# Performance work log

Hardware: AMD Instinct MI355X
Metric: run time of the kernel (lower is better)

The kernel has to match this reference:

```python
import jax, jax.numpy as jnp
import numpy as np

B, S, D, H = 4, 2048, 1024, 16
DEPTH = D // H  # 64


def setup_inputs() -> dict:
    key = jax.random.key(0)
    ks = jax.random.split(key, 11)
    scale = 1.0 / np.sqrt(D)
    inp = {
        "v": jax.random.normal(ks[0], (B, S, D), jnp.float32),
        "k": jax.random.normal(ks[1], (B, S, D), jnp.float32),
        "q": jax.random.normal(ks[2], (B, S, D), jnp.float32),
        # causal mask: 1.0 where attention is disallowed (strict upper triangle)
        "mask": jnp.triu(jnp.ones((S, S), jnp.float32), k=1)[None, None, :, :],
        "wq": jax.random.normal(ks[3], (D, D), jnp.float32) * scale,
        "bq": jnp.zeros((D,), jnp.float32),
        "wk": jax.random.normal(ks[4], (D, D), jnp.float32) * scale,
        "bk": jnp.zeros((D,), jnp.float32),
        "wv": jax.random.normal(ks[5], (D, D), jnp.float32) * scale,
        "bv": jnp.zeros((D,), jnp.float32),
        "wo": jax.random.normal(ks[6], (D, D), jnp.float32) * scale,
        "bo": jnp.zeros((D,), jnp.float32),
    }
    return inp


def _split_heads(x):
    # [B, S, D] -> [B, H, S, depth]
    b, s, _ = x.shape
    return x.reshape(b, s, H, DEPTH).transpose(0, 2, 1, 3)


def reference(v, k, q, mask, wq, bq, wk, bk, wv, bv, wo, bo):
    qh = _split_heads(q @ wq + bq)  # [B,H,S,depth]
    kh = _split_heads(k @ wk + bk)
    vh = _split_heads(v @ wv + bv)

    logits = jnp.einsum("bhqd,bhkd->bhqk", qh, kh) / jnp.sqrt(
        jnp.asarray(DEPTH, jnp.float32)
    )
    logits = logits + mask * -1e9
    attn = jax.nn.softmax(logits, axis=-1)  # [B,H,S,S]
    out = jnp.einsum("bhqk,bhkd->bhqd", attn, vh)
    out = out.transpose(0, 2, 1, 3).reshape(q.shape[0], -1, D)  # [B,S,D]
    return out @ wo + bo
```

## Files before the change

kernel.cpp:

```cpp
#include <hip/hip_runtime.h>

typedef _Float16 f16;
typedef _Float16 half8 __attribute__((ext_vector_type(8)));
typedef _Float16 half4v __attribute__((ext_vector_type(4)));
typedef _Float16 half2v __attribute__((ext_vector_type(2)));
typedef float f32x4 __attribute__((ext_vector_type(4)));

__device__ __forceinline__ void gl_lds16(const void* g, void* l) {
    __builtin_amdgcn_global_load_lds((const __attribute__((address_space(1))) void*)g,
                                     (__attribute__((address_space(3))) void*)l, 16, 0, 0);
}

__device__ __forceinline__ unsigned pack_f16(float a, float b) {
    union { half2v h; unsigned u; } un;
    un.h[0] = (f16)a; un.h[1] = (f16)b;
    return un.u;
}

__device__ __forceinline__ void prep_w_body(const float* __restrict__ W, f16* __restrict__ Wt)
{
    __shared__ float t[64][65];
    const int tid = threadIdx.x;
    const int tk = blockIdx.x * 64, tn = blockIdx.y * 64;
    const int rr = tid >> 4, cc = (tid & 15) * 4;
    #pragma unroll
    for (int j = 0; j < 4; ++j) {
        float4 v = *(const float4*)(W + (size_t)(tk + rr + j * 16) * 1024 + tn + cc);
        t[rr + j * 16][cc] = v.x; t[rr + j * 16][cc + 1] = v.y;
        t[rr + j * 16][cc + 2] = v.z; t[rr + j * 16][cc + 3] = v.w;
    }
    __syncthreads();
    const int n = tid >> 2, kc = (tid & 3) * 16;
    f16 o[16];
    #pragma unroll
    for (int j = 0; j < 16; ++j) o[j] = (f16)t[kc + j][n];
    f16* dst = Wt + (size_t)(tn + n) * 1024 + tk + kc;
    *(uint4*)dst = *(uint4*)o;
    *(uint4*)(dst + 8) = *(uint4*)(o + 8);
}

__global__ __launch_bounds__(256) void prep_w1(const float* __restrict__ W, f16* __restrict__ Wt)
{ prep_w_body(W, Wt); }

__global__ __launch_bounds__(256) void prep_w3(const float* __restrict__ w0,
    const float* __restrict__ w1, const float* __restrict__ w2, f16* __restrict__ Wt)
{
    const int z = blockIdx.z;
    const float* W = (z == 0) ? w0 : (z == 1) ? w1 : w2;
    prep_w_body(W, Wt + (size_t)z * 1024 * 1024);
}

__global__ __launch_bounds__(512, 2) void qkv_gemm(
    const float* __restrict__ Xq, const float* __restrict__ Xk, const float* __restrict__ Xv,
    const f16* __restrict__ Wt,
    const float* __restrict__ bqp, const float* __restrict__ bkp, const float* __restrict__ bvp,
    f16* __restrict__ qh, f16* __restrict__ kh, f16* __restrict__ vth)
{
    __shared__ __align__(16) f16 As[2][256 * 64];
    __shared__ __align__(16) f16 Bs[2][256 * 64];

    const int z = blockIdx.z;
    const float* X    = (z == 0) ? Xq : (z == 1) ? Xk : Xv;
    const float* bias = (z == 0) ? bqp : (z == 1) ? bkp : bvp;
    const f16*   W    = Wt + (size_t)z * 1024 * 1024;

    const int tid = threadIdx.x;
    const int lane = tid & 63;
    const int lane16 = lane & 15, quad = lane >> 4;
    const int wave = tid >> 6;
    const int wm = (wave & 1) * 128;
    const int wn = (wave >> 1) * 64;

    const int lin = blockIdx.x + 4 * blockIdx.y;
    const int xcd = lin & 7, t = lin >> 3;
    const int m0 = (((t >> 2) << 3) | xcd) * 256;
    const int n0 = (t & 3) * 256;

    const int srow = tid >> 3;
    const int sch  = tid & 7;
    const int swc  = sch ^ (srow & 7);

    const size_t xgbase = (size_t)(m0 + srow) * 1024 + sch * 8;
    const size_t wgbase = (size_t)(n0 + srow) * 1024 + swc * 8;
    const int wldsbase = (tid & 448) * 8;

    f32x4 acc[8][4] = {};

    {
        float4 xr[4][2];
        #pragma unroll
        for (int i = 0; i < 4; ++i) {
            xr[i][0] = *(const float4*)(X + xgbase + (size_t)i * 65536);
            xr[i][1] = *(const float4*)(X + xgbase + (size_t)i * 65536 + 4);
        }
        #pragma unroll
        for (int i = 0; i < 4; ++i)
            gl_lds16(W + wgbase + (size_t)i * 65536, Bs[0] + i * 4096 + wldsbase);
        asm volatile("s_waitcnt vmcnt(4)" ::: "memory");
        #pragma unroll
        for (int i = 0; i < 4; ++i) {
            half8 hx;
            hx[0] = (f16)xr[i][0].x; hx[1] = (f16)xr[i][0].y;
            hx[2] = (f16)xr[i][0].z; hx[3] = (f16)xr[i][0].w;
            hx[4] = (f16)xr[i][1].x; hx[5] = (f16)xr[i][1].y;
            hx[6] = (f16)xr[i][1].z; hx[7] = (f16)xr[i][1].w;
            *(half8*)(As[0] + i * 4096 + srow * 64 + swc * 8) = hx;
        }
        asm volatile("s_waitcnt vmcnt(0) lgkmcnt(0)" ::: "memory");
        __builtin_amdgcn_s_barrier();
        asm volatile("" ::: "memory");
    }

    for (int kt = 0; kt < 16; ++kt) {
        const int cur = kt & 1, nb = cur ^ 1;
        const bool pf = (kt + 1 < 16);
        const f16* Ab = As[cur];
        const f16* Bb = Bs[cur];

        float4 xr[4][2];
        if (pf) {
            const float* xs = X + xgbase + (kt + 1) * 64;
            #pragma unroll
            for (int i = 0; i < 4; ++i) {
                xr[i][0] = *(const float4*)(xs + (size_t)i * 65536);
                xr[i][1] = *(const float4*)(xs + (size_t)i * 65536 + 4);
            }
        }
        half8 af0[4][2], bf[4][2];
        #pragma unroll
        for (int i = 0; i < 4; ++i) {
            const int ra = wm + i * 16 + lane16;
            const int rb = wn + i * 16 + lane16;
            #pragma unroll
            for (int c = 0; c < 2; ++c) {
                af0[i][c] = *(const half8*)(Ab + ra * 64 + (((c * 4 + quad) ^ (ra & 7)) * 8));
                bf[i][c]  = *(const half8*)(Bb + rb * 64 + (((c * 4 + quad) ^ (rb & 7)) * 8));
            }
        }
        asm volatile("s_waitcnt lgkmcnt(0)" ::: "memory");
        __builtin_amdgcn_s_setprio(1);
        #pragma unroll
        for (int c = 0; c < 2; ++c)
            #pragma unroll
            for (int mi = 0; mi < 4; ++mi)
                #pragma unroll
                for (int ni = 0; ni < 4; ++ni)
                    acc[mi][ni] = __builtin_amdgcn_mfma_f32_16x16x32_f16(af0[mi][c], bf[ni][c], acc[mi][ni], 0, 0, 0);
        __builtin_amdgcn_s_setprio(0);
        asm volatile("" ::: "memory");
        __builtin_amdgcn_s_barrier();
        asm volatile("" ::: "memory");

        half8 af1[4][2];
        #pragma unroll
        for (int i = 0; i < 4; ++i) {
            const int ra = wm + 64 + i * 16 + lane16;
            #pragma unroll
            for (int c = 0; c < 2; ++c)
                af1[i][c] = *(const half8*)(Ab + ra * 64 + (((c * 4 + quad) ^ (ra & 7)) * 8));
        }
        if (pf) {
            const f16* ws = W + wgbase + (kt + 1) * 64;
            #pragma unroll
            for (int i = 0; i < 4; ++i)
                gl_lds16(ws + (size_t)i * 65536, Bs[nb] + i * 4096 + wldsbase);
            asm volatile("s_waitcnt vmcnt(4)" ::: "memory");
            #pragma unroll
            for (int i = 0; i < 4; ++i) {
                half8 hx;
                hx[0] = (f16)xr[i][0].x; hx[1] = (f16)xr[i][0].y;
                hx[2] = (f16)xr[i][0].z; hx[3] = (f16)xr[i][0].w;
                hx[4] = (f16)xr[i][1].x; hx[5] = (f16)xr[i][1].y;
                hx[6] = (f16)xr[i][1].z; hx[7] = (f16)xr[i][1].w;
                *(half8*)(As[nb] + i * 4096 + srow * 64 + swc * 8) = hx;
            }
        }
        asm volatile("s_waitcnt lgkmcnt(0)" ::: "memory");
        __builtin_amdgcn_s_setprio(1);
        #pragma unroll
        for (int c = 0; c < 2; ++c)
            #pragma unroll
            for (int mi = 0; mi < 4; ++mi)
                #pragma unroll
                for (int ni = 0; ni < 4; ++ni)
                    acc[4 + mi][ni] = __builtin_amdgcn_mfma_f32_16x16x32_f16(af1[mi][c], bf[ni][c], acc[4 + mi][ni], 0, 0, 0);
        __builtin_amdgcn_s_setprio(0);
        if (pf) asm volatile("s_waitcnt vmcnt(0)" ::: "memory");
        asm volatile("" ::: "memory");
        __builtin_amdgcn_s_barrier();
        asm volatile("" ::: "memory");
    }

    #pragma unroll
    for (int mi = 0; mi < 8; ++mi) {
        #pragma unroll
        for (int ni = 0; ni < 4; ++ni) {
            const int col = n0 + wn + ni * 16 + lane16;
            const float bval = bias[col];
            const int grow0 = m0 + wm + mi * 16 + quad * 4;
            if (z == 2) {
                const int b = grow0 >> 11, s0 = grow0 & 2047;
                const int h = col >> 6, d = col & 63;
                half4v p;
                #pragma unroll
                for (int r = 0; r < 4; ++r) p[r] = (f16)(acc[mi][ni][r] + bval);
                *(half4v*)(vth + (((size_t)b * 16 + h) * 64 + d) * 2048 + s0) = p;
            } else {
                f16* out = (z == 0) ? qh : kh;
                #pragma unroll
                for (int r = 0; r < 4; ++r)
                    out[(size_t)(grow0 + r) * 1024 + col] = (f16)(acc[mi][ni][r] + bval);
            }
        }
    }
}

__global__ __launch_bounds__(256, 2) void out_gemm(
    const f16* __restrict__ X, const f16* __restrict__ Wt,
    const float* __restrict__ bias, float* __restrict__ out)
{
    __shared__ __align__(16) f16 As[2][128 * 64];
    __shared__ __align__(16) f16 Bs[2][128 * 64];

    const int tid = threadIdx.x;
    const int lane = tid & 63;
    const int lane16 = lane & 15, quad = lane >> 4;
    const int wave = tid >> 6;
    const int wm = (wave >> 1) * 64, wn = (wave & 1) * 64;

    const int lin = blockIdx.x + 8 * blockIdx.y;
    const int xcd = lin & 7, t = lin >> 3;
    const int m0 = ((t >> 3) * 8 + xcd) * 128;
    const int n0 = (t & 7) * 128;

    const int wbase = tid & 192;
    const int srow = tid >> 3, schunk = tid & 7;
    const int swc = schunk ^ (srow & 7);

    f32x4 acc[4][4] = {};

    #pragma unroll
    for (int i = 0; i < 4; ++i) {
        gl_lds16(Wt + (size_t)(n0 + i * 32 + srow) * 1024 + swc * 8, Bs[0] + (size_t)(i * 256 + wbase) * 8);
        gl_lds16(X  + (size_t)(m0 + i * 32 + srow) * 1024 + swc * 8, As[0] + (size_t)(i * 256 + wbase) * 8);
    }

    for (int kt = 0; kt < 16; ++kt) {
        if (kt + 1 < 16) {
            const int nb = (kt + 1) & 1;
            const int k1 = (kt + 1) * 64;
            #pragma unroll
            for (int i = 0; i < 4; ++i) {
                gl_lds16(Wt + (size_t)(n0 + i * 32 + srow) * 1024 + k1 + swc * 8, Bs[nb] + (size_t)(i * 256 + wbase) * 8);
                gl_lds16(X  + (size_t)(m0 + i * 32 + srow) * 1024 + k1 + swc * 8, As[nb] + (size_t)(i * 256 + wbase) * 8);
            }
            asm volatile("s_waitcnt vmcnt(8)" ::: "memory");
        } else {
            asm volatile("s_waitcnt vmcnt(0)" ::: "memory");
        }
        __builtin_amdgcn_s_barrier();
        asm volatile("" ::: "memory");

        const f16* Ab = As[kt & 1];
        const f16* Bb = Bs[kt & 1];
        half8 af[4][2], bf[4][2];
        #pragma unroll
        for (int i = 0; i < 4; ++i) {
            const int ra = wm + i * 16 + lane16;
            const int rb = wn + i * 16 + lane16;
            #pragma unroll
            for (int c = 0; c < 2; ++c) {
                af[i][c] = *(const half8*)(Ab + ra * 64 + (((c * 4 + quad) ^ (ra & 7)) * 8));
                bf[i][c] = *(const half8*)(Bb + rb * 64 + (((c * 4 + quad) ^ (rb & 7)) * 8));
            }
        }
        #pragma unroll
        for (int c = 0; c < 2; ++c)
            #pragma unroll
            for (int mi = 0; mi < 4; ++mi)
                #pragma unroll
                for (int ni = 0; ni < 4; ++ni)
                    acc[mi][ni] = __builtin_amdgcn_mfma_f32_16x16x32_f16(af[mi][c], bf[ni][c], acc[mi][ni], 0, 0, 0);

        asm volatile("" ::: "memory");
        __builtin_amdgcn_s_barrier();
        asm volatile("" ::: "memory");
    }

    #pragma unroll
    for (int mi = 0; mi < 4; ++mi) {
        #pragma unroll
        for (int ni = 0; ni < 4; ++ni) {
            const int col = n0 + wn + ni * 16 + lane16;
            const float bval = bias[col];
            const int grow0 = m0 + wm + mi * 16 + quad * 4;
            #pragma unroll
            for (int r = 0; r < 4; ++r)
                out[(size_t)(grow0 + r) * 1024 + col] = acc[mi][ni][r] + bval;
        }
    }
}

__global__ __launch_bounds__(256, 4) void attn_kernel(
    const f16* __restrict__ qh, const f16* __restrict__ kh,
    const f16* __restrict__ vt, f16* __restrict__ at)
{
    __shared__ __align__(16) f16 Ks[2][64 * 64];
    __shared__ __align__(16) f16 Vts[2][64 * 64];

    const int tid = threadIdx.x;
    const int lane = tid & 63, wave = tid >> 6;
    const int lane16 = lane & 15, quad = lane >> 4;
    const int wbase = tid & 192;
    const int l3 = lane16 & 7;
    const int srow = tid >> 3, schunk = tid & 7;

    const int lin = blockIdx.x + 16 * blockIdx.y;
    const int xcd = lin & 7, t = lin >> 3;
    const int bh = xcd + 8 * (t & 7);
    const int qi = 15 - (t >> 3);
    const int b = bh >> 4, h = bh & 15;

    const f16* qp = qh + (size_t)b * 2048 * 1024 + h * 64;
    const f16* kp = kh + (size_t)b * 2048 * 1024 + h * 64;
    const f16* vtp = vt + (size_t)bh * 64 * 2048;

    const int qb = 128 * qi;
    const int qrow0 = qb + wave * 32;
    const int ntiles = qb / 64 + 2;
    const int qmax = qrow0 + 31;

    #pragma unroll
    for (int i = 0; i < 2; ++i) {
        const int row = i * 32 + srow;
        const int sw = (schunk ^ (row & 7)) * 8;
        gl_lds16(kp + (size_t)row * 1024 + sw, Ks[0] + (size_t)(i * 256 + wbase) * 8);
        gl_lds16(vtp + (size_t)row * 2048 + sw, Vts[0] + (size_t)(i * 256 + wbase) * 8);
    }

    half8 aq[2][2];
    #pragma unroll
    for (int mt = 0; mt < 2; ++mt)
        #pragma unroll
        for (int c = 0; c < 2; ++c)
            aq[mt][c] = *(const half8*)(qp + (size_t)(qrow0 + mt * 16 + lane16) * 1024 + c * 32 + quad * 8);

    f32x4 o[4][2] = {};
    float lp[2] = {0.0f, 0.0f};

    for (int kt = 0; kt < ntiles; ++kt) {
        if (kt + 1 < ntiles) {
            const int nb = (kt + 1) & 1;
            const int k1 = (kt + 1) * 64;
            #pragma unroll
            for (int i = 0; i < 2; ++i) {
                const int row = i * 32 + srow;
                const int sw = (schunk ^ (row & 7)) * 8;
                gl_lds16(kp + (size_t)(k1 + row) * 1024 + sw, Ks[nb] + (size_t)(i * 256 + wbase) * 8);
                gl_lds16(vtp + (size_t)row * 2048 + k1 + sw, Vts[nb] + (size_t)(i * 256 + wbase) * 8);
            }
            asm volatile("s_waitcnt vmcnt(4)" ::: "memory");
        } else {
            asm volatile("s_waitcnt vmcnt(0)" ::: "memory");
        }
        __builtin_amdgcn_s_barrier();
        asm volatile("" ::: "memory");

        const int k0 = kt * 64;
        if (k0 <= qmax) {
            const f16* Kb = Ks[kt & 1];
            const f16* Vb = Vts[kt & 1];
            f32x4 sT[4][2];
            #pragma unroll
            for (int sub = 0; sub < 4; ++sub) {
                const int kr = sub * 16 + lane16;
                const half8 ak0 = *(const half8*)(Kb + kr * 64 + ((quad ^ l3) * 8));
                const half8 ak1 = *(const half8*)(Kb + kr * 64 + (((4 + quad) ^ l3) * 8));
                #pragma unroll
                for (int mt = 0; mt < 2; ++mt) {
                    f32x4 z = {};
                    z = __builtin_amdgcn_mfma_f32_16x16x32_f16(ak0, aq[mt][0], z, 0, 0, 0);
                    z = __builtin_amdgcn_mfma_f32_16x16x32_f16(ak1, aq[mt][1], z, 0, 0, 0);
                    sT[sub][mt] = z;
                }
            }
            const bool needmask = (k0 + 63 > qrow0);
            if (needmask) {
                #pragma unroll
                for (int sub = 0; sub < 4; ++sub)
                    #pragma unroll
                    for (int mt = 0; mt < 2; ++mt)
                        #pragma unroll
                        for (int r = 0; r < 4; ++r) {
                            const int key = k0 + sub * 16 + quad * 4 + r;
                            const int qi2 = qrow0 + mt * 16 + lane16;
                            if (key > qi2) sT[sub][mt][r] = -1e30f;
                        }
            }

            half8 bp[2][2];
            #pragma unroll
            for (int mt = 0; mt < 2; ++mt) {
                unsigned pk01[4], pk23[4];
                #pragma unroll
                for (int sub = 0; sub < 4; ++sub) {
                    float p[4];
                    #pragma unroll
                    for (int r = 0; r < 4; ++r) {
                        const float x = fmaf(sT[sub][mt][r], 0.18033688011112042f, -5.770780163555852f);
                        float e;
                        asm("v_exp_f32 %0, %1" : "=v"(e) : "v"(x));
                        p[r] = e;
                        lp[mt] += e;
                    }
                    pk01[sub] = pack_f16(p[0], p[1]);
                    pk23[sub] = pack_f16(p[2], p[3]);
                }
                #pragma unroll
                for (int c = 0; c < 2; ++c) {
                    unsigned a0 = pk01[2 * c], b0 = pk01[2 * c + 1];
                    unsigned a1 = pk23[2 * c], b1 = pk23[2 * c + 1];
                    asm("v_permlane32_swap_b32 %0, %1" : "+v"(a0), "+v"(b0));
                    asm("v_permlane16_swap_b32 %0, %1" : "+v"(a0), "+v"(b0));
                    asm("v_permlane32_swap_b32 %0, %1" : "+v"(a1), "+v"(b1));
                    asm("v_permlane16_swap_b32 %0, %1" : "+v"(a1), "+v"(b1));
                    union { unsigned u[4]; half8 h8; } un;
                    un.u[0] = a0; un.u[1] = a1; un.u[2] = b0; un.u[3] = b1;
                    bp[c][mt] = un.h8;
                }
            }

            #pragma unroll
            for (int nt = 0; nt < 4; ++nt) {
                const int dr = nt * 16 + lane16;
                const half8 av0 = *(const half8*)(Vb + dr * 64 + ((quad ^ l3) * 8));
                const half8 av1 = *(const half8*)(Vb + dr * 64 + (((4 + quad) ^ l3) * 8));
                #pragma unroll
                for (int mt = 0; mt < 2; ++mt) {
                    o[nt][mt] = __builtin_amdgcn_mfma_f32_16x16x32_f16(av0, bp[0][mt], o[nt][mt], 0, 0, 0);
                    o[nt][mt] = __builtin_amdgcn_mfma_f32_16x16x32_f16(av1, bp[1][mt], o[nt][mt], 0, 0, 0);
                }
            }
        }
        asm volatile("" ::: "memory");
        __builtin_amdgcn_s_barrier();
        asm volatile("" ::: "memory");
    }

    #pragma unroll
    for (int mt = 0; mt < 2; ++mt) {
        float red = lp[mt];
        red += __shfl_xor(red, 16);
        red += __shfl_xor(red, 32);
        const float inv = 1.0f / red;
        const int sr = qrow0 + mt * 16 + lane16;
        f16* dst = at + ((size_t)b * 2048 + sr) * 1024 + h * 64 + quad * 4;
        #pragma unroll
        for (int nt = 0; nt < 4; ++nt) {
            half4v p;
            #pragma unroll
            for (int r = 0; r < 4; ++r) p[r] = (f16)(o[nt][mt][r] * inv);
            *(half4v*)(dst + nt * 16) = p;
        }
    }
}

extern "C" void kernel_launch(void* const* d_in, const int* in_sizes, int n_in,
                              void* d_out, int out_size, void* d_ws, size_t ws_size,
                              hipStream_t stream)
{
    const float* v  = (const float*)d_in[0];
    const float* k  = (const float*)d_in[1];
    const float* q  = (const float*)d_in[2];
    const float* wq = (const float*)d_in[4];
    const float* bq = (const float*)d_in[5];
    const float* wk = (const float*)d_in[6];
    const float* bk = (const float*)d_in[7];
    const float* wv = (const float*)d_in[8];
    const float* bv = (const float*)d_in[9];
    const float* wo = (const float*)d_in[10];
    const float* bo = (const float*)d_in[11];

    f16* qh = (f16*)d_ws;
    f16* kh = qh + (size_t)8 * 1024 * 1024;
    f16* vt = kh + (size_t)8 * 1024 * 1024;
    f16* at = vt + (size_t)8 * 1024 * 1024;

    f16* wT = (f16*)d_out;
    f16* woT = qh;

    prep_w3<<<dim3(16, 16, 3), 256, 0, stream>>>(wq, wk, wv, wT);

    qkv_gemm<<<dim3(4, 32, 3), 512, 0, stream>>>(q, k, v, wT, bq, bk, bv, qh, kh, vt);

    attn_kernel<<<dim3(16, 64), 256, 0, stream>>>(qh, kh, vt, at);

    prep_w1<<<dim3(16, 16), 256, 0, stream>>>(wo, woT);
    out_gemm<<<dim3(8, 64), 256, 0, stream>>>(at, woT, bo, (float*)d_out);
}
```

Baseline: 329.1 us.

## Split QKV GEMM k-step into four MFMA phases with interleaved prefetch

Restructures the qkv_gemm main loop from two MFMA phases into four quadrant phases (A rows × B column halves). The W global-to-LDS prefetch and the X prefetch loads and f16 conversions are spread across these phases with extra barriers, and the launch bound drops from 2 to 1 block per CU, which frees more registers. The aim is to overlap memory traffic with MFMA work and lower register pressure per phase. It adds more barriers per iteration and may lose occupancy-based latency hiding.

```diff
diff --git a/kernel.cpp b/kernel.cpp
--- a/kernel.cpp
+++ b/kernel.cpp
@@ -50,7 +50,7 @@
     prep_w_body(W, Wt + (size_t)z * 1024 * 1024);
 }
 
-__global__ __launch_bounds__(512, 2) void qkv_gemm(
+__global__ __launch_bounds__(512, 1) void qkv_gemm(
     const float* __restrict__ Xq, const float* __restrict__ Xk, const float* __restrict__ Xv,
     const f16* __restrict__ Wt,
     const float* __restrict__ bqp, const float* __restrict__ bkp, const float* __restrict__ bvp,
@@ -67,6 +67,7 @@
     const int tid = threadIdx.x;
     const int lane = tid & 63;
     const int lane16 = lane & 15, quad = lane >> 4;
+    const int l3 = lane16 & 7;
     const int wave = tid >> 6;
     const int wm = (wave & 1) * 128;
     const int wn = (wave >> 1) * 64;
@@ -87,18 +88,18 @@
     f32x4 acc[8][4] = {};
 
     {
+        #pragma unroll
+        for (int i = 0; i < 4; ++i)
+            gl_lds16(W + wgbase + (size_t)i * 65536, Bs[0] + i * 4096 + wldsbase);
         float4 xr[4][2];
         #pragma unroll
         for (int i = 0; i < 4; ++i) {
             xr[i][0] = *(const float4*)(X + xgbase + (size_t)i * 65536);
             xr[i][1] = *(const float4*)(X + xgbase + (size_t)i * 65536 + 4);
         }
-        #pragma unroll
-        for (int i = 0; i < 4; ++i)
-            gl_lds16(W + wgbase + (size_t)i * 65536, Bs[0] + i * 4096 + wldsbase);
         asm volatile("s_waitcnt vmcnt(4)" ::: "memory");
         #pragma unroll
-        for (int i = 0; i < 4; ++i) {
+        for (int i = 0; i < 2; ++i) {
             half8 hx;
             hx[0] = (f16)xr[i][0].x; hx[1] = (f16)xr[i][0].y;
             hx[2] = (f16)xr[i][0].z; hx[3] = (f16)xr[i][0].w;
@@ -106,7 +107,17 @@
             hx[6] = (f16)xr[i][1].z; hx[7] = (f16)xr[i][1].w;
             *(half8*)(As[0] + i * 4096 + srow * 64 + swc * 8) = hx;
         }
-        asm volatile("s_waitcnt vmcnt(0) lgkmcnt(0)" ::: "memory");
+        asm volatile("s_waitcnt vmcnt(0)" ::: "memory");
+        #pragma unroll
+        for (int i = 2; i < 4; ++i) {
+            half8 hx;
+            hx[0] = (f16)xr[i][0].x; hx[1] = (f16)xr[i][0].y;
+            hx[2] = (f16)xr[i][0].z; hx[3] = (f16)xr[i][0].w;
+            hx[4] = (f16)xr[i][1].x; hx[5] = (f16)xr[i][1].y;
+            hx[6] = (f16)xr[i][1].z; hx[7] = (f16)xr[i][1].w;
+            *(half8*)(As[0] + i * 4096 + srow * 64 + swc * 8) = hx;
+        }
+        asm volatile("s_waitcnt lgkmcnt(0)" ::: "memory");
         __builtin_amdgcn_s_barrier();
         asm volatile("" ::: "memory");
     }
@@ -116,27 +127,31 @@
         const bool pf = (kt + 1 < 16);
         const f16* Ab = As[cur];
         const f16* Bb = Bs[cur];
-
+        const f16* wsrc = W + wgbase + (kt + 1) * 64;
+        const float* xsrc = X + xgbase + (kt + 1) * 64;
         float4 xr[4][2];
-        if (pf) {
-            const float* xs = X + xgbase + (kt + 1) * 64;
-            #pragma unroll
-            for (int i = 0; i < 4; ++i) {
-                xr[i][0] = *(const float4*)(xs + (size_t)i * 65536);
-                xr[i][1] = *(const float4*)(xs + (size_t)i * 65536 + 4);
-            }
-        }
-        half8 af0[4][2], bf[4][2];
+
+        half8 af[4][2], bf01[2][2], bf23[2][2];
         #pragma unroll
         for (int i = 0; i < 4; ++i) {
             const int ra = wm + i * 16 + lane16;
+            #pragma unroll
+            for (int c = 0; c < 2; ++c)
+                af[i][c] = *(const half8*)(Ab + ra * 64 + (((c * 4 + quad) ^ l3) * 8));
+        }
+        #pragma unroll
+        for (int i = 0; i < 2; ++i) {
             const int rb = wn + i * 16 + lane16;
             #pragma unroll
-            for (int c = 0; c < 2; ++c) {
-                af0[i][c] = *(const half8*)(Ab + ra * 64 + (((c * 4 + quad) ^ (ra & 7)) * 8));
-                bf[i][c]  = *(const half8*)(Bb + rb * 64 + (((c * 4 + quad) ^ (rb & 7)) * 8));
-            }
-        }
+            for (int c = 0; c < 2; ++c)
+                bf01[i][c] = *(const half8*)(Bb + rb * 64 + (((c * 4 + quad) ^ l3) * 8));
+        }
+        if (pf) {
+            #pragma unroll
+            for (int i = 0; i < 4; ++i)
+                gl_lds16(wsrc + (size_t)i * 65536, Bs[nb] + i * 4096 + wldsbase);
+        }
+        __builtin_amdgcn_s_barrier();
         asm volatile("s_waitcnt lgkmcnt(0)" ::: "memory");
         __builtin_amdgcn_s_setprio(1);
         #pragma unroll
@@ -144,29 +159,54 @@
             #pragma unroll
             for (int mi = 0; mi < 4; ++mi)
                 #pragma unroll
-                for (int ni = 0; ni < 4; ++ni)
-                    acc[mi][ni] = __builtin_amdgcn_mfma_f32_16x16x32_f16(af0[mi][c], bf[ni][c], acc[mi][ni], 0, 0, 0);
+                for (int ni = 0; ni < 2; ++ni)
+                    acc[mi][ni] = __builtin_amdgcn_mfma_f32_16x16x32_f16(af[mi][c], bf01[ni][c], acc[mi][ni], 0, 0, 0);
         __builtin_amdgcn_s_setprio(0);
         asm volatile("" ::: "memory");
         __builtin_amdgcn_s_barrier();
         asm volatile("" ::: "memory");
 
-        half8 af1[4][2];
+        #pragma unroll
+        for (int i = 0; i < 2; ++i) {
+            const int rb = wn + (i + 2) * 16 + lane16;
+            #pragma unroll
+            for (int c = 0; c < 2; ++c)
+                bf23[i][c] = *(const half8*)(Bb + rb * 64 + (((c * 4 + quad) ^ l3) * 8));
+        }
+        if (pf) {
+            #pragma unroll
+            for (int i = 0; i < 4; ++i) {
+                xr[i][0] = *(const float4*)(xsrc + (size_t)i * 65536);
+                xr[i][1] = *(const float4*)(xsrc + (size_t)i * 65536 + 4);
+            }
+        }
+        __builtin_amdgcn_s_barrier();
+        asm volatile("s_waitcnt lgkmcnt(0)" ::: "memory");
+        __builtin_amdgcn_s_setprio(1);
+        #pragma unroll
+        for (int c = 0; c < 2; ++c)
+            #pragma unroll
+            for (int mi = 0; mi < 4; ++mi)
+                #pragma unroll
+                for (int ni = 0; ni < 2; ++ni)
+                    acc[mi][ni + 2] = __builtin_amdgcn_mfma_f32_16x16x32_f16(af[mi][c], bf23[ni][c], acc[mi][ni + 2], 0, 0, 0);
+        __builtin_amdgcn_s_setprio(0);
+        asm volatile("" ::: "memory");
+        __builtin_amdgcn_s_barrier();
+        asm volatile("" ::: "memory");
+
+        half8 ag[4][2];
         #pragma unroll
         for (int i = 0; i < 4; ++i) {
             const int ra = wm + 64 + i * 16 + lane16;
             #pragma unroll
             for (int c = 0; c < 2; ++c)
-                af1[i][c] = *(const half8*)(Ab + ra * 64 + (((c * 4 + quad) ^ (ra & 7)) * 8));
+                ag[i][c] = *(const half8*)(Ab + ra * 64 + (((c * 4 + quad) ^ l3) * 8));
         }
         if (pf) {
-            const f16* ws = W + wgbase + (kt + 1) * 64;
-            #pragma unroll
-            for (int i = 0; i < 4; ++i)
-                gl_lds16(ws + (size_t)i * 65536, Bs[nb] + i * 4096 + wldsbase);
             asm volatile("s_waitcnt vmcnt(4)" ::: "memory");
             #pragma unroll
-            for (int i = 0; i < 4; ++i) {
+            for (int i = 0; i < 2; ++i) {
                 half8 hx;
                 hx[0] = (f16)xr[i][0].x; hx[1] = (f16)xr[i][0].y;
                 hx[2] = (f16)xr[i][0].z; hx[3] = (f16)xr[i][0].w;
@@ -175,6 +215,7 @@
                 *(half8*)(As[nb] + i * 4096 + srow * 64 + swc * 8) = hx;
             }
         }
+        __builtin_amdgcn_s_barrier();
         asm volatile("s_waitcnt lgkmcnt(0)" ::: "memory");
         __builtin_amdgcn_s_setprio(1);
         #pragma unroll
@@ -182,10 +223,36 @@
             #pragma unroll
             for (int mi = 0; mi < 4; ++mi)
                 #pragma unroll
-                for (int ni = 0; ni < 4; ++ni)
-                    acc[4 + mi][ni] = __builtin_amdgcn_mfma_f32_16x16x32_f16(af1[mi][c], bf[ni][c], acc[4 + mi][ni], 0, 0, 0);
+                for (int ni = 0; ni < 2; ++ni)
+                    acc[mi + 4][ni] = __builtin_amdgcn_mfma_f32_16x16x32_f16(ag[mi][c], bf01[ni][c], acc[mi + 4][ni], 0, 0, 0);
         __builtin_amdgcn_s_setprio(0);
-        if (pf) asm volatile("s_waitcnt vmcnt(0)" ::: "memory");
+        asm volatile("" ::: "memory");
+        __builtin_amdgcn_s_barrier();
+        asm volatile("" ::: "memory");
+
+        if (pf) {
+            asm volatile("s_waitcnt vmcnt(0)" ::: "memory");
+            #pragma unroll
+            for (int i = 2; i < 4; ++i) {
+                half8 hx;
+                hx[0] = (f16)xr[i][0].x; hx[1] = (f16)xr[i][0].y;
+                hx[2] = (f16)xr[i][0].z; hx[3] = (f16)xr[i][0].w;
+                hx[4] = (f16)xr[i][1].x; hx[5] = (f16)xr[i][1].y;
+                hx[6] = (f16)xr[i][1].z; hx[7] = (f16)xr[i][1].w;
+                *(half8*)(As[nb] + i * 4096 + srow * 64 + swc * 8) = hx;
+            }
+            asm volatile("s_waitcnt lgkmcnt(0)" ::: "memory");
+        }
+        __builtin_amdgcn_s_barrier();
+        __builtin_amdgcn_s_setprio(1);
+        #pragma unroll
+        for (int c = 0; c < 2; ++c)
+            #pragma unroll
+            for (int mi = 0; mi < 4; ++mi)
+                #pragma unroll
+                for (int ni = 0; ni < 2; ++ni)
+                    acc[mi + 4][ni + 2] = __builtin_amdgcn_mfma_f32_16x16x32_f16(ag[mi][c], bf23[ni][c], acc[mi + 4][ni + 2], 0, 0, 0);
+        __builtin_amdgcn_s_setprio(0);
         asm volatile("" ::: "memory");
         __builtin_amdgcn_s_barrier();
         asm volatile("" ::: "memory");
```

Result: slower. 340.9 us (+3.6%).
